# Optimization experiments

Hardware: AMD Instinct MI355X
Metric: run time of the kernel (lower is better)

Reference implementation:

```python
import jax, jax.numpy as jnp
import numpy as np

B, L, D, H = 4, 1024, 1024, 16
DK = D // H


def setup_inputs() -> dict:
    key = jax.random.key(0)
    ks = jax.random.split(key, 5)
    s = 1.0 / np.sqrt(D)  # roughly nn.Linear init scale
    return {
        "x": jax.random.normal(ks[0], (B, L, D), dtype=jnp.float32),
        "Wq": jax.random.normal(ks[1], (D, D), dtype=jnp.float32) * s,
        "bq": jnp.zeros((D,), dtype=jnp.float32),
        "Wk": jax.random.normal(ks[2], (D, D), dtype=jnp.float32) * s,
        "bk": jnp.zeros((D,), dtype=jnp.float32),
        "Wv": jax.random.normal(ks[3], (D, D), dtype=jnp.float32) * s,
        "bv": jnp.zeros((D,), dtype=jnp.float32),
        "Wo": jax.random.normal(ks[4], (D, D), dtype=jnp.float32) * s,
        "bo": jnp.zeros((D,), dtype=jnp.float32),
    }


def reference(x, Wq, bq, Wk, bk, Wv, bv, Wo, bo):
    b, l, d = x.shape
    # torch Linear: y = x @ W.T + b
    q = (x @ Wq.T + bq).reshape(b, l, H, DK).transpose(0, 2, 1, 3)  # [B,H,L,DK]
    k = (x @ Wk.T + bk).reshape(b, l, H, DK).transpose(0, 2, 1, 3)
    v = (x @ Wv.T + bv).reshape(b, l, H, DK).transpose(0, 2, 1, 3)
    scores = jnp.einsum("bhqd,bhkd->bhqk", q, k) / jnp.sqrt(jnp.float32(DK))
    attn = jax.nn.softmax(scores, axis=-1)  # dropout p=0 -> identity
    head_out = jnp.einsum("bhqk,bhkd->bhqd", attn, v)  # [B,H,L,DK]
    merged = head_out.transpose(0, 2, 1, 3).reshape(b, l, d)  # [B,L,D]
    out = merged @ Wo.T + bo
    # DeCov loss over head outputs
    U = merged.reshape(b * l, d)
    U = U - U.mean(axis=0, keepdims=True)
    C = (U.T @ U) / jnp.float32(b * l)
    decov = 0.5 * (jnp.sum(C * C) - jnp.sum(jnp.diag(C) ** 2))
    return (out, decov)
```

## Files before the change

kernel.cpp:

```cpp
#include <hip/hip_runtime.h>
#include <cstdint>
#include <cstddef>

typedef short v4s __attribute__((ext_vector_type(4)));
typedef short v8s __attribute__((ext_vector_type(8)));
typedef float v4f __attribute__((ext_vector_type(4)));

__device__ __forceinline__ short f2bf(float f) {
    union { float f; unsigned u; } x; x.f = f;
    unsigned r = (x.u + 0x7FFFu + ((x.u >> 16) & 1u)) >> 16;
    return (short)(unsigned short)r;
}
__device__ __forceinline__ float bf2f(short h) {
    union { unsigned u; float f; } x; x.u = ((unsigned)(unsigned short)h) << 16;
    return x.f;
}

__device__ __forceinline__ void gld16(const void* g, void* l) {
    __builtin_amdgcn_global_load_lds((const __attribute__((address_space(1))) void*)g,
                                     (__attribute__((address_space(3))) void*)l, 16, 0, 0);
}

__global__ __launch_bounds__(256) void cvt_bf16(
    const float* __restrict__ x, const float* __restrict__ wq, const float* __restrict__ wk,
    const float* __restrict__ wv, const float* __restrict__ wo,
    short* __restrict__ xb, short* __restrict__ wqb, short* __restrict__ wkb,
    short* __restrict__ wvb, short* __restrict__ wob)
{
    int bid = blockIdx.x;
    const float* src; short* dst; size_t base;
    if (bid < 4096)      { src = x;  dst = xb;  base = (size_t)bid * 1024; }
    else if (bid < 5120) { src = wq; dst = wqb; base = (size_t)(bid - 4096) * 1024; }
    else if (bid < 6144) { src = wk; dst = wkb; base = (size_t)(bid - 5120) * 1024; }
    else if (bid < 7168) { src = wv; dst = wvb; base = (size_t)(bid - 6144) * 1024; }
    else                 { src = wo; dst = wob; base = (size_t)(bid - 7168) * 1024; }
    size_t idx = base + (size_t)threadIdx.x * 4;
    v4f v = *(const v4f*)(src + idx);
    v4s o;
    o[0] = f2bf(v[0]); o[1] = f2bf(v[1]); o[2] = f2bf(v[2]); o[3] = f2bf(v[3]);
    *(v4s*)(dst + idx) = o;
}

__global__ __launch_bounds__(256) void gemm_qkv(
    const short* __restrict__ xb,
    const short* __restrict__ wq, const short* __restrict__ wk, const short* __restrict__ wv,
    const float* __restrict__ bq, const float* __restrict__ bk, const float* __restrict__ bv,
    short* __restrict__ qo, short* __restrict__ ko, short* __restrict__ vto)
{
    __shared__ __align__(16) short At[128 * 32];
    __shared__ __align__(16) short Bt[128 * 32];
    const int K = 1024;
    const int mode = blockIdx.z;
    const short* W = (mode == 0) ? wq : (mode == 1) ? wk : wv;
    const float* bias = (mode == 0) ? bq : (mode == 1) ? bk : bv;
    const int m0 = blockIdx.y * 128, n0 = blockIdx.x * 128;
    const int tid = threadIdx.x, wave = tid >> 6, lane = tid & 63;
    const int quad = lane >> 4, ll = lane & 15;
    const int wr = wave >> 1, wc = wave & 1;
    const v4f zero4 = {0.f, 0.f, 0.f, 0.f};
    v4f acc[4][4];
    for (int i = 0; i < 4; ++i) for (int j = 0; j < 4; ++j) acc[i][j] = zero4;

    for (int k0 = 0; k0 < K; k0 += 32) {
        __syncthreads();
#pragma unroll
        for (int c = 0; c < 2; ++c) {
            int chb = (wave * 2 + c) * 64;
            int ch = chb + lane;
            int row = ch >> 2, col8 = (ch & 3) * 8;
            gld16(xb + (size_t)(m0 + row) * K + k0 + col8, &At[chb * 8]);
            gld16(W  + (size_t)(n0 + row) * K + k0 + col8, &Bt[chb * 8]);
        }
        __syncthreads();
        v8s af[4], bfr[4];
#pragma unroll
        for (int i = 0; i < 4; ++i) af[i]  = *(const v8s*)&At[(wr * 64 + i * 16 + ll) * 32 + quad * 8];
#pragma unroll
        for (int j = 0; j < 4; ++j) bfr[j] = *(const v8s*)&Bt[(wc * 64 + j * 16 + ll) * 32 + quad * 8];
#pragma unroll
        for (int i = 0; i < 4; ++i)
#pragma unroll
            for (int j = 0; j < 4; ++j)
                acc[i][j] = __builtin_amdgcn_mfma_f32_16x16x32_bf16(af[i], bfr[j], acc[i][j], 0, 0, 0);
    }

    const float scale = (mode == 0) ? 0.125f : 1.0f;
#pragma unroll
    for (int j = 0; j < 4; ++j) {
        int n = n0 + wc * 64 + j * 16 + ll;
        float bb = bias[n];
        int hh = n >> 6, dk = n & 63;
#pragma unroll
        for (int i = 0; i < 4; ++i) {
            int mbase = m0 + wr * 64 + i * 16 + quad * 4;
#pragma unroll
            for (int r = 0; r < 4; ++r) {
                int m = mbase + r;
                int b = m >> 10, li = m & 1023;
                short h = f2bf((acc[i][j][r] + bb) * scale);
                if (mode == 0)
                    qo[(((size_t)(b * 16 + hh) * 1024 + li) << 6) + dk] = h;
                else if (mode == 1)
                    ko[(((size_t)(b * 16 + hh) * 1024 + li) << 6) + dk] = h;
                else
                    vto[(((size_t)(b * 16 + hh) * 64 + dk) << 10) + li] = h;
            }
        }
    }
}

__global__ __launch_bounds__(256) void gemm_out(
    const short* __restrict__ A, const short* __restrict__ W,
    const float* __restrict__ bias, float* __restrict__ out)
{
    __shared__ __align__(16) short At[128 * 32];
    __shared__ __align__(16) short Bt[128 * 32];
    const int K = 1024;
    const int m0 = blockIdx.y * 128, n0 = blockIdx.x * 128;
    const int tid = threadIdx.x, wave = tid >> 6, lane = tid & 63;
    const int quad = lane >> 4, ll = lane & 15;
    const int wr = wave >> 1, wc = wave & 1;
    const v4f zero4 = {0.f, 0.f, 0.f, 0.f};
    v4f acc[4][4];
    for (int i = 0; i < 4; ++i) for (int j = 0; j < 4; ++j) acc[i][j] = zero4;

    for (int k0 = 0; k0 < K; k0 += 32) {
        __syncthreads();
#pragma unroll
        for (int c = 0; c < 2; ++c) {
            int chb = (wave * 2 + c) * 64;
            int ch = chb + lane;
            int row = ch >> 2, col8 = (ch & 3) * 8;
            gld16(A + (size_t)(m0 + row) * K + k0 + col8, &At[chb * 8]);
            gld16(W + (size_t)(n0 + row) * K + k0 + col8, &Bt[chb * 8]);
        }
        __syncthreads();
        v8s af[4], bfr[4];
#pragma unroll
        for (int i = 0; i < 4; ++i) af[i]  = *(const v8s*)&At[(wr * 64 + i * 16 + ll) * 32 + quad * 8];
#pragma unroll
        for (int j = 0; j < 4; ++j) bfr[j] = *(const v8s*)&Bt[(wc * 64 + j * 16 + ll) * 32 + quad * 8];
#pragma unroll
        for (int i = 0; i < 4; ++i)
#pragma unroll
            for (int j = 0; j < 4; ++j)
                acc[i][j] = __builtin_amdgcn_mfma_f32_16x16x32_bf16(af[i], bfr[j], acc[i][j], 0, 0, 0);
    }

#pragma unroll
    for (int j = 0; j < 4; ++j) {
        int n = n0 + wc * 64 + j * 16 + ll;
        float bb = bias[n];
#pragma unroll
        for (int i = 0; i < 4; ++i) {
            int mbase = m0 + wr * 64 + i * 16 + quad * 4;
#pragma unroll
            for (int r = 0; r < 4; ++r) {
                int m = mbase + r;
                out[(size_t)m * 1024 + n] = acc[i][j][r] + bb;
            }
        }
    }
}

__global__ __launch_bounds__(256) void attn_flash(
    const short* __restrict__ qb, const short* __restrict__ kb, const short* __restrict__ vtb,
    float* __restrict__ merged, short* __restrict__ mergedh, float* __restrict__ colsum)
{
    __shared__ __align__(16) short Kt[64 * 64];
    __shared__ __align__(16) short Vt[64 * 64];
    __shared__ __align__(16) short Pt[4 * 16 * 68];
    const int bh = blockIdx.y, qt = blockIdx.x;
    const int tid = threadIdx.x, wave = tid >> 6, lane = tid & 63;
    const int quad = lane >> 4, ll = lane & 15;
    const short* qp = qb  + (size_t)bh * 1024 * 64;
    const short* kp = kb  + (size_t)bh * 1024 * 64;
    const short* vp = vtb + (size_t)bh * 64 * 1024;

    const int qrow = qt * 64 + wave * 16 + ll;
    v8s qa0 = *(const v8s*)(qp + (size_t)qrow * 64 + quad * 8);
    v8s qa1 = *(const v8s*)(qp + (size_t)qrow * 64 + 32 + quad * 8);

    const v4f zero4 = {0.f, 0.f, 0.f, 0.f};
    v4f oacc[4];
    for (int nt = 0; nt < 4; ++nt) oacc[nt] = zero4;
    float lsum[4] = {0.f, 0.f, 0.f, 0.f};
    short* pw = &Pt[wave * 16 * 68];

    for (int jt = 0; jt < 16; ++jt) {
        __syncthreads();
#pragma unroll
        for (int c = 0; c < 2; ++c) {
            int chb = (wave * 2 + c) * 64;
            int ch = chb + lane;
            int row = ch >> 3;
            int gi = ((ch & 7) ^ (row & 7)) * 8;
            gld16(kp + (size_t)(jt * 64 + row) * 64 + gi, &Kt[chb * 8]);
            gld16(vp + (size_t)row * 1024 + jt * 64 + gi, &Vt[chb * 8]);
        }
        __syncthreads();

        v4f sacc[4];
#pragma unroll
        for (int nt = 0; nt < 4; ++nt) {
            int n = nt * 16 + ll;
            int g0 = (quad ^ (n & 7)) * 8;
            int g1 = ((4 + quad) ^ (n & 7)) * 8;
            v8s b0 = *(const v8s*)&Kt[n * 64 + g0];
            v8s b1 = *(const v8s*)&Kt[n * 64 + g1];
            v4f s = zero4;
            s = __builtin_amdgcn_mfma_f32_16x16x32_bf16(qa0, b0, s, 0, 0, 0);
            s = __builtin_amdgcn_mfma_f32_16x16x32_bf16(qa1, b1, s, 0, 0, 0);
            sacc[nt] = s;
        }
#pragma unroll
        for (int nt = 0; nt < 4; ++nt) {
#pragma unroll
            for (int r = 0; r < 4; ++r) {
                float e = __expf(sacc[nt][r]);
                lsum[r] += e;
                pw[(quad * 4 + r) * 68 + nt * 16 + ll] = f2bf(e);
            }
        }
        v4s p00 = *(const v4s*)&pw[ll * 68 + quad * 8];
        v4s p01 = *(const v4s*)&pw[ll * 68 + quad * 8 + 4];
        v4s p10 = *(const v4s*)&pw[ll * 68 + 32 + quad * 8];
        v4s p11 = *(const v4s*)&pw[ll * 68 + 32 + quad * 8 + 4];
        v8s pa0 = __builtin_shufflevector(p00, p01, 0, 1, 2, 3, 4, 5, 6, 7);
        v8s pa1 = __builtin_shufflevector(p10, p11, 0, 1, 2, 3, 4, 5, 6, 7);
#pragma unroll
        for (int nt = 0; nt < 4; ++nt) {
            int n = nt * 16 + ll;
            int g0 = (quad ^ (n & 7)) * 8;
            int g1 = ((4 + quad) ^ (n & 7)) * 8;
            v8s v0 = *(const v8s*)&Vt[n * 64 + g0];
            v8s v1 = *(const v8s*)&Vt[n * 64 + g1];
            oacc[nt] = __builtin_amdgcn_mfma_f32_16x16x32_bf16(pa0, v0, oacc[nt], 0, 0, 0);
            oacc[nt] = __builtin_amdgcn_mfma_f32_16x16x32_bf16(pa1, v1, oacc[nt], 0, 0, 0);
        }
    }

    float linv[4];
#pragma unroll
    for (int r = 0; r < 4; ++r) {
        float s = lsum[r];
        s += __shfl_xor(s, 1); s += __shfl_xor(s, 2);
        s += __shfl_xor(s, 4); s += __shfl_xor(s, 8);
        linv[r] = 1.0f / s;
    }
    const int b = bh >> 4, h = bh & 15;
    float csum[4] = {0.f, 0.f, 0.f, 0.f};
#pragma unroll
    for (int r = 0; r < 4; ++r) {
        int li = qt * 64 + wave * 16 + quad * 4 + r;
        size_t rowoff = ((size_t)(b * 1024 + li)) * 1024 + h * 64;
#pragma unroll
        for (int nt = 0; nt < 4; ++nt) {
            int d = nt * 16 + ll;
            float v = oacc[nt][r] * linv[r];
            merged[rowoff + d] = v;
            mergedh[rowoff + d] = f2bf(v);
            csum[nt] += v;
        }
    }
#pragma unroll
    for (int nt = 0; nt < 4; ++nt) {
        csum[nt] += __shfl_xor(csum[nt], 16);
        csum[nt] += __shfl_xor(csum[nt], 32);
    }
    if (quad == 0) {
#pragma unroll
        for (int nt = 0; nt < 4; ++nt)
            atomicAdd(&colsum[h * 64 + nt * 16 + ll], csum[nt]);
    }
}

__global__ __launch_bounds__(256) void center_tr(
    const float* __restrict__ merged, const float* __restrict__ colsum,
    short* __restrict__ uth, short* __restrict__ utl)
{
    __shared__ short Hh[64][72];
    __shared__ short Hl[64][72];
    const int d0 = blockIdx.x * 64, m0 = blockIdx.y * 64;
    const int t = threadIdx.x;
    const int r0 = t >> 4, c4 = (t & 15) * 4;
    float mu[4];
#pragma unroll
    for (int e = 0; e < 4; ++e) mu[e] = colsum[d0 + c4 + e] * (1.0f / 4096.0f);
    for (int rr = 0; rr < 64; rr += 16) {
        int m = m0 + rr + r0;
        v4f v = *(const v4f*)(merged + (size_t)m * 1024 + d0 + c4);
#pragma unroll
        for (int e = 0; e < 4; ++e) {
            float u = v[e] - mu[e];
            short h = f2bf(u);
            Hh[c4 + e][rr + r0] = h;
            Hl[c4 + e][rr + r0] = f2bf(u - bf2f(h));
        }
    }
    __syncthreads();
    const int d = t >> 2, mg = (t & 3) * 16;
    v8s a0, a1, b0, b1;
#pragma unroll
    for (int e = 0; e < 8; ++e) {
        a0[e] = Hh[d][mg + e]; a1[e] = Hh[d][mg + 8 + e];
        b0[e] = Hl[d][mg + e]; b1[e] = Hl[d][mg + 8 + e];
    }
    size_t off = (size_t)(d0 + d) * 4096 + m0 + mg;
    *(v8s*)(uth + off) = a0; *(v8s*)(uth + off + 8) = a1;
    *(v8s*)(utl + off) = b0; *(v8s*)(utl + off + 8) = b1;
}

__global__ __launch_bounds__(256) void gemm_decov(
    const short* __restrict__ uth, const short* __restrict__ utl, float* __restrict__ cpart)
{
    int p = blockIdx.x, I = 0, rem = p;
    while (rem >= 16 - I) { rem -= 16 - I; ++I; }
    const int J = I + rem;
    const int kbase = blockIdx.y * 512;
    __shared__ __align__(16) short Ah[64 * 32], Al[64 * 32], Bh[64 * 32], Bl[64 * 32];
    const int tid = threadIdx.x;
    const int wave = tid >> 6, lane = tid & 63;
    const int quad = lane >> 4, ll = lane & 15;
    const int wr = wave >> 1, wc = wave & 1;
    const v4f zero4 = {0.f, 0.f, 0.f, 0.f};
    v4f acc[2][2];
    for (int i = 0; i < 2; ++i) for (int j = 0; j < 2; ++j) acc[i][j] = zero4;

    for (int kk = 0; kk < 512; kk += 32) {
        int k0 = kbase + kk;
        __syncthreads();
        {
            int ch = wave * 64 + lane;
            int row = ch >> 2, col8 = (ch & 3) * 8;
            gld16(uth + (size_t)(I * 64 + row) * 4096 + k0 + col8, &Ah[wave * 512]);
            gld16(utl + (size_t)(I * 64 + row) * 4096 + k0 + col8, &Al[wave * 512]);
            gld16(uth + (size_t)(J * 64 + row) * 4096 + k0 + col8, &Bh[wave * 512]);
            gld16(utl + (size_t)(J * 64 + row) * 4096 + k0 + col8, &Bl[wave * 512]);
        }
        __syncthreads();
        v8s ah[2], al[2], bh[2], bl[2];
#pragma unroll
        for (int i = 0; i < 2; ++i) {
            int ro = (wr * 32 + i * 16 + ll) * 32 + quad * 8;
            ah[i] = *(const v8s*)&Ah[ro];
            al[i] = *(const v8s*)&Al[ro];
        }
#pragma unroll
        for (int j = 0; j < 2; ++j) {
            int ro = (wc * 32 + j * 16 + ll) * 32 + quad * 8;
            bh[j] = *(const v8s*)&Bh[ro];
            bl[j] = *(const v8s*)&Bl[ro];
        }
#pragma unroll
        for (int i = 0; i < 2; ++i)
#pragma unroll
            for (int j = 0; j < 2; ++j) {
                acc[i][j] = __builtin_amdgcn_mfma_f32_16x16x32_bf16(ah[i], bh[j], acc[i][j], 0, 0, 0);
                acc[i][j] = __builtin_amdgcn_mfma_f32_16x16x32_bf16(ah[i], bl[j], acc[i][j], 0, 0, 0);
                acc[i][j] = __builtin_amdgcn_mfma_f32_16x16x32_bf16(al[i], bh[j], acc[i][j], 0, 0, 0);
            }
    }

    float* dst = cpart + ((size_t)blockIdx.y * 136 + p) * 4096;
#pragma unroll
    for (int i = 0; i < 2; ++i)
#pragma unroll
        for (int j = 0; j < 2; ++j)
#pragma unroll
            for (int r = 0; r < 4; ++r) {
                int gi2 = wr * 32 + i * 16 + quad * 4 + r;
                int gj2 = wc * 32 + j * 16 + ll;
                dst[gi2 * 64 + gj2] = acc[i][j][r];
            }
}

__global__ __launch_bounds__(256) void decov_reduce(const float* __restrict__ cpart, float* __restrict__ dsum) {
    int p = blockIdx.x, I = 0, rem = p;
    while (rem >= 16 - I) { rem -= 16 - I; ++I; }
    const int J = I + rem;
    const int t = threadIdx.x;
    __shared__ float wsums[4];
    float s = 0.f;
    for (int e = t; e < 4096; e += 256) {
        float c = 0.f;
#pragma unroll
        for (int kc = 0; kc < 8; ++kc) c += cpart[((size_t)kc * 136 + p) * 4096 + e];
        int gi = I * 64 + (e >> 6), gj = J * 64 + (e & 63);
        if (gi != gj) s += c * c;
    }
    if (I < J) s *= 2.f;
    s += __shfl_xor(s, 1); s += __shfl_xor(s, 2); s += __shfl_xor(s, 4);
    s += __shfl_xor(s, 8); s += __shfl_xor(s, 16); s += __shfl_xor(s, 32);
    if ((t & 63) == 0) wsums[t >> 6] = s;
    __syncthreads();
    if (t == 0) dsum[p] = wsums[0] + wsums[1] + wsums[2] + wsums[3];
}

__global__ __launch_bounds__(256) void decov_final(const float* __restrict__ dsum, float* __restrict__ out) {
    const int t = threadIdx.x;
    __shared__ float wsums[4];
    float s = (t < 136) ? dsum[t] : 0.f;
    s += __shfl_xor(s, 1); s += __shfl_xor(s, 2); s += __shfl_xor(s, 4);
    s += __shfl_xor(s, 8); s += __shfl_xor(s, 16); s += __shfl_xor(s, 32);
    if ((t & 63) == 0) wsums[t >> 6] = s;
    __syncthreads();
    if (t == 0) {
        float tot = wsums[0] + wsums[1] + wsums[2] + wsums[3];
        out[4194304] = 0.5f * tot / (4096.0f * 4096.0f);
    }
}

extern "C" void kernel_launch(void* const* d_in, const int* in_sizes, int n_in,
                              void* d_out, int out_size, void* d_ws, size_t ws_size,
                              hipStream_t stream) {
    const float* x  = (const float*)d_in[0];
    const float* Wq = (const float*)d_in[1];
    const float* bq = (const float*)d_in[2];
    const float* Wk = (const float*)d_in[3];
    const float* bk = (const float*)d_in[4];
    const float* Wv = (const float*)d_in[5];
    const float* bv = (const float*)d_in[6];
    const float* Wo = (const float*)d_in[7];
    const float* bo = (const float*)d_in[8];
    float* out = (float*)d_out;
    char* ws = (char*)d_ws;
    const size_t MB = 1ull << 20;
    short* xb      = (short*)(ws);
    short* wqb     = (short*)(ws + 8  * MB);
    short* wkb     = (short*)(ws + 10 * MB);
    short* wvb     = (short*)(ws + 12 * MB);
    short* wob     = (short*)(ws + 14 * MB);
    short* qb      = (short*)(ws + 16 * MB);
    short* kb      = (short*)(ws + 24 * MB);
    short* vtb     = (short*)(ws + 32 * MB);
    float* merged  = (float*)(ws + 40 * MB);
    short* mergedh = (short*)(ws + 56 * MB);
    short* uth     = (short*)(ws + 65 * MB);
    short* utl     = (short*)(ws + 73 * MB);
    float* dsum    = (float*)(ws + 81 * MB);
    float* colsum  = (float*)(ws + 81 * MB + 4096);
    float* cpart   = (float*)(ws);

    hipMemsetAsync(colsum, 0, 4096, stream);
    hipLaunchKernelGGL(cvt_bf16, dim3(8192), dim3(256), 0, stream,
                       x, Wq, Wk, Wv, Wo, xb, wqb, wkb, wvb, wob);
    hipLaunchKernelGGL(gemm_qkv, dim3(8, 32, 3), dim3(256), 0, stream,
                       xb, wqb, wkb, wvb, bq, bk, bv, qb, kb, vtb);
    hipLaunchKernelGGL(attn_flash, dim3(16, 64), dim3(256), 0, stream,
                       qb, kb, vtb, merged, mergedh, colsum);
    hipLaunchKernelGGL(gemm_out, dim3(8, 32), dim3(256), 0, stream,
                       mergedh, wob, bo, out);
    hipLaunchKernelGGL(center_tr, dim3(16, 64), dim3(256), 0, stream,
                       merged, colsum, uth, utl);
    hipLaunchKernelGGL(gemm_decov, dim3(136, 8), dim3(256), 0, stream, uth, utl, cpart);
    hipLaunchKernelGGL(decov_reduce, dim3(136), dim3(256), 0, stream, cpart, dsum);
    hipLaunchKernelGGL(decov_final, dim3(1), dim3(256), 0, stream, dsum, out);
}
```

Before: 246.1 us.

## Merge out-proj and centering kernels, double attention rows per wave, fold memset

Three changes. The colsum memset is folded into the bf16 conversion kernel. The attention kernel now gives each wave 32 query rows, two 16-row MFMA tiles sharing each K/V LDS fragment, which halves the grid and reuses K/V loads. The output projection GEMM and the centering/transpose kernel are merged into a single launch that dispatches on block index, so they run concurrently. This cuts launch count and improves K/V reuse, at the cost of higher register pressure in attention and fewer attention blocks to fill the GPU.

```diff
diff --git a/kernel.cpp b/kernel.cpp
--- a/kernel.cpp
+++ b/kernel.cpp
@@ -25,7 +25,7 @@
     const float* __restrict__ x, const float* __restrict__ wq, const float* __restrict__ wk,
     const float* __restrict__ wv, const float* __restrict__ wo,
     short* __restrict__ xb, short* __restrict__ wqb, short* __restrict__ wkb,
-    short* __restrict__ wvb, short* __restrict__ wob)
+    short* __restrict__ wvb, short* __restrict__ wob, float* __restrict__ colsum)
 {
     int bid = blockIdx.x;
     const float* src; short* dst; size_t base;
@@ -39,6 +39,10 @@
     v4s o;
     o[0] = f2bf(v[0]); o[1] = f2bf(v[1]); o[2] = f2bf(v[2]); o[3] = f2bf(v[3]);
     *(v4s*)(dst + idx) = o;
+    if (bid == 0) {
+        v4f z = {0.f, 0.f, 0.f, 0.f};
+        *(v4f*)(colsum + (size_t)threadIdx.x * 4) = z;
+    }
 }
 
 __global__ __launch_bounds__(256) void gemm_qkv(
@@ -109,67 +113,13 @@
     }
 }
 
-__global__ __launch_bounds__(256) void gemm_out(
-    const short* __restrict__ A, const short* __restrict__ W,
-    const float* __restrict__ bias, float* __restrict__ out)
-{
-    __shared__ __align__(16) short At[128 * 32];
-    __shared__ __align__(16) short Bt[128 * 32];
-    const int K = 1024;
-    const int m0 = blockIdx.y * 128, n0 = blockIdx.x * 128;
-    const int tid = threadIdx.x, wave = tid >> 6, lane = tid & 63;
-    const int quad = lane >> 4, ll = lane & 15;
-    const int wr = wave >> 1, wc = wave & 1;
-    const v4f zero4 = {0.f, 0.f, 0.f, 0.f};
-    v4f acc[4][4];
-    for (int i = 0; i < 4; ++i) for (int j = 0; j < 4; ++j) acc[i][j] = zero4;
-
-    for (int k0 = 0; k0 < K; k0 += 32) {
-        __syncthreads();
-#pragma unroll
-        for (int c = 0; c < 2; ++c) {
-            int chb = (wave * 2 + c) * 64;
-            int ch = chb + lane;
-            int row = ch >> 2, col8 = (ch & 3) * 8;
-            gld16(A + (size_t)(m0 + row) * K + k0 + col8, &At[chb * 8]);
-            gld16(W + (size_t)(n0 + row) * K + k0 + col8, &Bt[chb * 8]);
-        }
-        __syncthreads();
-        v8s af[4], bfr[4];
-#pragma unroll
-        for (int i = 0; i < 4; ++i) af[i]  = *(const v8s*)&At[(wr * 64 + i * 16 + ll) * 32 + quad * 8];
-#pragma unroll
-        for (int j = 0; j < 4; ++j) bfr[j] = *(const v8s*)&Bt[(wc * 64 + j * 16 + ll) * 32 + quad * 8];
-#pragma unroll
-        for (int i = 0; i < 4; ++i)
-#pragma unroll
-            for (int j = 0; j < 4; ++j)
-                acc[i][j] = __builtin_amdgcn_mfma_f32_16x16x32_bf16(af[i], bfr[j], acc[i][j], 0, 0, 0);
-    }
-
-#pragma unroll
-    for (int j = 0; j < 4; ++j) {
-        int n = n0 + wc * 64 + j * 16 + ll;
-        float bb = bias[n];
-#pragma unroll
-        for (int i = 0; i < 4; ++i) {
-            int mbase = m0 + wr * 64 + i * 16 + quad * 4;
-#pragma unroll
-            for (int r = 0; r < 4; ++r) {
-                int m = mbase + r;
-                out[(size_t)m * 1024 + n] = acc[i][j][r] + bb;
-            }
-        }
-    }
-}
-
 __global__ __launch_bounds__(256) void attn_flash(
     const short* __restrict__ qb, const short* __restrict__ kb, const short* __restrict__ vtb,
     float* __restrict__ merged, short* __restrict__ mergedh, float* __restrict__ colsum)
 {
     __shared__ __align__(16) short Kt[64 * 64];
     __shared__ __align__(16) short Vt[64 * 64];
-    __shared__ __align__(16) short Pt[4 * 16 * 68];
+    __shared__ __align__(16) short Pt[4 * 32 * 68];
     const int bh = blockIdx.y, qt = blockIdx.x;
     const int tid = threadIdx.x, wave = tid >> 6, lane = tid & 63;
     const int quad = lane >> 4, ll = lane & 15;
@@ -177,15 +127,20 @@
     const short* kp = kb  + (size_t)bh * 1024 * 64;
     const short* vp = vtb + (size_t)bh * 64 * 1024;
 
-    const int qrow = qt * 64 + wave * 16 + ll;
-    v8s qa0 = *(const v8s*)(qp + (size_t)qrow * 64 + quad * 8);
-    v8s qa1 = *(const v8s*)(qp + (size_t)qrow * 64 + 32 + quad * 8);
+    v8s qa[2][2];
+#pragma unroll
+    for (int mi = 0; mi < 2; ++mi) {
+        int qrow = qt * 128 + wave * 32 + mi * 16 + ll;
+        qa[mi][0] = *(const v8s*)(qp + (size_t)qrow * 64 + quad * 8);
+        qa[mi][1] = *(const v8s*)(qp + (size_t)qrow * 64 + 32 + quad * 8);
+    }
 
     const v4f zero4 = {0.f, 0.f, 0.f, 0.f};
-    v4f oacc[4];
-    for (int nt = 0; nt < 4; ++nt) oacc[nt] = zero4;
-    float lsum[4] = {0.f, 0.f, 0.f, 0.f};
-    short* pw = &Pt[wave * 16 * 68];
+    v4f oacc[2][4];
+    for (int mi = 0; mi < 2; ++mi) for (int nt = 0; nt < 4; ++nt) oacc[mi][nt] = zero4;
+    float lsum[2][4];
+    for (int mi = 0; mi < 2; ++mi) for (int r = 0; r < 4; ++r) lsum[mi][r] = 0.f;
+    short* pw = &Pt[wave * 32 * 68];
 
     for (int jt = 0; jt < 16; ++jt) {
         __syncthreads();
@@ -200,7 +155,7 @@
         }
         __syncthreads();
 
-        v4f sacc[4];
+        v4f sacc[2][4];
 #pragma unroll
         for (int nt = 0; nt < 4; ++nt) {
             int n = nt * 16 + ll;
@@ -208,26 +163,34 @@
             int g1 = ((4 + quad) ^ (n & 7)) * 8;
             v8s b0 = *(const v8s*)&Kt[n * 64 + g0];
             v8s b1 = *(const v8s*)&Kt[n * 64 + g1];
-            v4f s = zero4;
-            s = __builtin_amdgcn_mfma_f32_16x16x32_bf16(qa0, b0, s, 0, 0, 0);
-            s = __builtin_amdgcn_mfma_f32_16x16x32_bf16(qa1, b1, s, 0, 0, 0);
-            sacc[nt] = s;
-        }
-#pragma unroll
-        for (int nt = 0; nt < 4; ++nt) {
-#pragma unroll
-            for (int r = 0; r < 4; ++r) {
-                float e = __expf(sacc[nt][r]);
-                lsum[r] += e;
-                pw[(quad * 4 + r) * 68 + nt * 16 + ll] = f2bf(e);
-            }
-        }
-        v4s p00 = *(const v4s*)&pw[ll * 68 + quad * 8];
-        v4s p01 = *(const v4s*)&pw[ll * 68 + quad * 8 + 4];
-        v4s p10 = *(const v4s*)&pw[ll * 68 + 32 + quad * 8];
-        v4s p11 = *(const v4s*)&pw[ll * 68 + 32 + quad * 8 + 4];
-        v8s pa0 = __builtin_shufflevector(p00, p01, 0, 1, 2, 3, 4, 5, 6, 7);
-        v8s pa1 = __builtin_shufflevector(p10, p11, 0, 1, 2, 3, 4, 5, 6, 7);
+#pragma unroll
+            for (int mi = 0; mi < 2; ++mi) {
+                v4f s = zero4;
+                s = __builtin_amdgcn_mfma_f32_16x16x32_bf16(qa[mi][0], b0, s, 0, 0, 0);
+                s = __builtin_amdgcn_mfma_f32_16x16x32_bf16(qa[mi][1], b1, s, 0, 0, 0);
+                sacc[mi][nt] = s;
+            }
+        }
+#pragma unroll
+        for (int mi = 0; mi < 2; ++mi)
+#pragma unroll
+            for (int nt = 0; nt < 4; ++nt)
+#pragma unroll
+                for (int r = 0; r < 4; ++r) {
+                    float e = __expf(sacc[mi][nt][r]);
+                    lsum[mi][r] += e;
+                    pw[(mi * 16 + quad * 4 + r) * 68 + nt * 16 + ll] = f2bf(e);
+                }
+        v8s pa[2][2];
+#pragma unroll
+        for (int mi = 0; mi < 2; ++mi) {
+            v4s p00 = *(const v4s*)&pw[(mi * 16 + ll) * 68 + quad * 8];
+            v4s p01 = *(const v4s*)&pw[(mi * 16 + ll) * 68 + quad * 8 + 4];
+            v4s p10 = *(const v4s*)&pw[(mi * 16 + ll) * 68 + 32 + quad * 8];
+            v4s p11 = *(const v4s*)&pw[(mi * 16 + ll) * 68 + 32 + quad * 8 + 4];
+            pa[mi][0] = __builtin_shufflevector(p00, p01, 0, 1, 2, 3, 4, 5, 6, 7);
+            pa[mi][1] = __builtin_shufflevector(p10, p11, 0, 1, 2, 3, 4, 5, 6, 7);
+        }
 #pragma unroll
         for (int nt = 0; nt < 4; ++nt) {
             int n = nt * 16 + ll;
@@ -235,32 +198,38 @@
             int g1 = ((4 + quad) ^ (n & 7)) * 8;
             v8s v0 = *(const v8s*)&Vt[n * 64 + g0];
             v8s v1 = *(const v8s*)&Vt[n * 64 + g1];
-            oacc[nt] = __builtin_amdgcn_mfma_f32_16x16x32_bf16(pa0, v0, oacc[nt], 0, 0, 0);
-            oacc[nt] = __builtin_amdgcn_mfma_f32_16x16x32_bf16(pa1, v1, oacc[nt], 0, 0, 0);
-        }
-    }
-
-    float linv[4];
-#pragma unroll
-    for (int r = 0; r < 4; ++r) {
-        float s = lsum[r];
-        s += __shfl_xor(s, 1); s += __shfl_xor(s, 2);
-        s += __shfl_xor(s, 4); s += __shfl_xor(s, 8);
-        linv[r] = 1.0f / s;
-    }
+#pragma unroll
+            for (int mi = 0; mi < 2; ++mi) {
+                oacc[mi][nt] = __builtin_amdgcn_mfma_f32_16x16x32_bf16(pa[mi][0], v0, oacc[mi][nt], 0, 0, 0);
+                oacc[mi][nt] = __builtin_amdgcn_mfma_f32_16x16x32_bf16(pa[mi][1], v1, oacc[mi][nt], 0, 0, 0);
+            }
+        }
+    }
+
     const int b = bh >> 4, h = bh & 15;
     float csum[4] = {0.f, 0.f, 0.f, 0.f};
 #pragma unroll
-    for (int r = 0; r < 4; ++r) {
-        int li = qt * 64 + wave * 16 + quad * 4 + r;
-        size_t rowoff = ((size_t)(b * 1024 + li)) * 1024 + h * 64;
-#pragma unroll
-        for (int nt = 0; nt < 4; ++nt) {
-            int d = nt * 16 + ll;
-            float v = oacc[nt][r] * linv[r];
-            merged[rowoff + d] = v;
-            mergedh[rowoff + d] = f2bf(v);
-            csum[nt] += v;
+    for (int mi = 0; mi < 2; ++mi) {
+        float linv[4];
+#pragma unroll
+        for (int r = 0; r < 4; ++r) {
+            float s = lsum[mi][r];
+            s += __shfl_xor(s, 1); s += __shfl_xor(s, 2);
+            s += __shfl_xor(s, 4); s += __shfl_xor(s, 8);
+            linv[r] = 1.0f / s;
+        }
+#pragma unroll
+        for (int r = 0; r < 4; ++r) {
+            int li = qt * 128 + wave * 32 + mi * 16 + quad * 4 + r;
+            size_t rowoff = ((size_t)(b * 1024 + li)) * 1024 + h * 64;
+#pragma unroll
+            for (int nt = 0; nt < 4; ++nt) {
+                int d = nt * 16 + ll;
+                float v = oacc[mi][nt][r] * linv[r];
+                merged[rowoff + d] = v;
+                mergedh[rowoff + d] = f2bf(v);
+                csum[nt] += v;
+            }
         }
     }
 #pragma unroll
@@ -275,40 +244,96 @@
     }
 }
 
-__global__ __launch_bounds__(256) void center_tr(
+__global__ __launch_bounds__(256) void post_attn(
+    const short* __restrict__ A, const short* __restrict__ W, const float* __restrict__ bias,
+    float* __restrict__ out,
     const float* __restrict__ merged, const float* __restrict__ colsum,
     short* __restrict__ uth, short* __restrict__ utl)
 {
-    __shared__ short Hh[64][72];
-    __shared__ short Hl[64][72];
-    const int d0 = blockIdx.x * 64, m0 = blockIdx.y * 64;
-    const int t = threadIdx.x;
-    const int r0 = t >> 4, c4 = (t & 15) * 4;
-    float mu[4];
-#pragma unroll
-    for (int e = 0; e < 4; ++e) mu[e] = colsum[d0 + c4 + e] * (1.0f / 4096.0f);
-    for (int rr = 0; rr < 64; rr += 16) {
-        int m = m0 + rr + r0;
-        v4f v = *(const v4f*)(merged + (size_t)m * 1024 + d0 + c4);
-#pragma unroll
-        for (int e = 0; e < 4; ++e) {
-            float u = v[e] - mu[e];
-            short h = f2bf(u);
-            Hh[c4 + e][rr + r0] = h;
-            Hl[c4 + e][rr + r0] = f2bf(u - bf2f(h));
-        }
-    }
-    __syncthreads();
-    const int d = t >> 2, mg = (t & 3) * 16;
-    v8s a0, a1, b0, b1;
-#pragma unroll
-    for (int e = 0; e < 8; ++e) {
-        a0[e] = Hh[d][mg + e]; a1[e] = Hh[d][mg + 8 + e];
-        b0[e] = Hl[d][mg + e]; b1[e] = Hl[d][mg + 8 + e];
-    }
-    size_t off = (size_t)(d0 + d) * 4096 + m0 + mg;
-    *(v8s*)(uth + off) = a0; *(v8s*)(uth + off + 8) = a1;
-    *(v8s*)(utl + off) = b0; *(v8s*)(utl + off + 8) = b1;
+    __shared__ __align__(16) char smem[18432];
+    const int bid = blockIdx.x;
+    const int tid = threadIdx.x;
+    if (bid < 256) {
+        short* At = (short*)smem;
+        short* Bt = (short*)(smem + 8192);
+        const int K = 1024;
+        const int n0 = (bid & 7) * 128, m0 = (bid >> 3) * 128;
+        const int wave = tid >> 6, lane = tid & 63;
+        const int quad = lane >> 4, ll = lane & 15;
+        const int wr = wave >> 1, wc = wave & 1;
+        const v4f zero4 = {0.f, 0.f, 0.f, 0.f};
+        v4f acc[4][4];
+        for (int i = 0; i < 4; ++i) for (int j = 0; j < 4; ++j) acc[i][j] = zero4;
+
+        for (int k0 = 0; k0 < K; k0 += 32) {
+            __syncthreads();
+#pragma unroll
+            for (int c = 0; c < 2; ++c) {
+                int chb = (wave * 2 + c) * 64;
+                int ch = chb + lane;
+                int row = ch >> 2, col8 = (ch & 3) * 8;
+                gld16(A + (size_t)(m0 + row) * K + k0 + col8, &At[chb * 8]);
+                gld16(W + (size_t)(n0 + row) * K + k0 + col8, &Bt[chb * 8]);
+            }
+            __syncthreads();
+            v8s af[4], bfr[4];
+#pragma unroll
+            for (int i = 0; i < 4; ++i) af[i]  = *(const v8s*)&At[(wr * 64 + i * 16 + ll) * 32 + quad * 8];
+#pragma unroll
+            for (int j = 0; j < 4; ++j) bfr[j] = *(const v8s*)&Bt[(wc * 64 + j * 16 + ll) * 32 + quad * 8];
+#pragma unroll
+            for (int i = 0; i < 4; ++i)
+#pragma unroll
+                for (int j = 0; j < 4; ++j)
+                    acc[i][j] = __builtin_amdgcn_mfma_f32_16x16x32_bf16(af[i], bfr[j], acc[i][j], 0, 0, 0);
+        }
+
+#pragma unroll
+        for (int j = 0; j < 4; ++j) {
+            int n = n0 + wc * 64 + j * 16 + ll;
+            float bb = bias[n];
+#pragma unroll
+            for (int i = 0; i < 4; ++i) {
+                int mbase = m0 + wr * 64 + i * 16 + quad * 4;
+#pragma unroll
+                for (int r = 0; r < 4; ++r) {
+                    int m = mbase + r;
+                    out[(size_t)m * 1024 + n] = acc[i][j][r] + bb;
+                }
+            }
+        }
+    } else {
+        short (*Hh)[72] = (short(*)[72])smem;
+        short (*Hl)[72] = (short(*)[72])(smem + 9216);
+        const int cid = bid - 256;
+        const int d0 = (cid & 15) * 64, m0 = (cid >> 4) * 64;
+        const int r0 = tid >> 4, c4 = (tid & 15) * 4;
+        float mu[4];
+#pragma unroll
+        for (int e = 0; e < 4; ++e) mu[e] = colsum[d0 + c4 + e] * (1.0f / 4096.0f);
+        for (int rr = 0; rr < 64; rr += 16) {
+            int m = m0 + rr + r0;
+            v4f v = *(const v4f*)(merged + (size_t)m * 1024 + d0 + c4);
+#pragma unroll
+            for (int e = 0; e < 4; ++e) {
+                float u = v[e] - mu[e];
+                short h = f2bf(u);
+                Hh[c4 + e][rr + r0] = h;
+                Hl[c4 + e][rr + r0] = f2bf(u - bf2f(h));
+            }
+        }
+        __syncthreads();
+        const int d = tid >> 2, mg = (tid & 3) * 16;
+        v8s a0, a1, b0, b1;
+#pragma unroll
+        for (int e = 0; e < 8; ++e) {
+            a0[e] = Hh[d][mg + e]; a1[e] = Hh[d][mg + 8 + e];
+            b0[e] = Hl[d][mg + e]; b1[e] = Hl[d][mg + 8 + e];
+        }
+        size_t off = (size_t)(d0 + d) * 4096 + m0 + mg;
+        *(v8s*)(uth + off) = a0; *(v8s*)(uth + off + 8) = a1;
+        *(v8s*)(utl + off) = b0; *(v8s*)(utl + off + 8) = b1;
+    }
 }
 
 __global__ __launch_bounds__(256) void gemm_decov(
@@ -442,17 +467,14 @@
     float* colsum  = (float*)(ws + 81 * MB + 4096);
     float* cpart   = (float*)(ws);
 
-    hipMemsetAsync(colsum, 0, 4096, stream);
     hipLaunchKernelGGL(cvt_bf16, dim3(8192), dim3(256), 0, stream,
-                       x, Wq, Wk, Wv, Wo, xb, wqb, wkb, wvb, wob);
+                       x, Wq, Wk, Wv, Wo, xb, wqb, wkb, wvb, wob, colsum);
     hipLaunchKernelGGL(gemm_qkv, dim3(8, 32, 3), dim3(256), 0, stream,
                        xb, wqb, wkb, wvb, bq, bk, bv, qb, kb, vtb);
-    hipLaunchKernelGGL(attn_flash, dim3(16, 64), dim3(256), 0, stream,
+    hipLaunchKernelGGL(attn_flash, dim3(8, 64), dim3(256), 0, stream,
                        qb, kb, vtb, merged, mergedh, colsum);
-    hipLaunchKernelGGL(gemm_out, dim3(8, 32), dim3(256), 0, stream,
-                       mergedh, wob, bo, out);
-    hipLaunchKernelGGL(center_tr, dim3(16, 64), dim3(256), 0, stream,
-                       merged, colsum, uth, utl);
+    hipLaunchKernelGGL(post_attn, dim3(1280), dim3(256), 0, stream,
+                       mergedh, wob, bo, out, merged, colsum, uth, utl);
     hipLaunchKernelGGL(gemm_decov, dim3(136, 8), dim3(256), 0, stream, uth, utl, cpart);
     hipLaunchKernelGGL(decov_reduce, dim3(136), dim3(256), 0, stream, cpart, dsum);
     hipLaunchKernelGGL(decov_final, dim3(1), dim3(256), 0, stream, dsum, out);
```

New measurement: 236.3 us. 1.04x faster.
